# Optimization experiments

Measured on AMD Instinct MI355X. Metric: run time of the kernel, lower is better.

The kernel has to match this reference:

```python
import jax, jax.numpy as jnp
import numpy as np

B, S, H, D = 4, 2048, 16, 64
CAUSAL = True
NEG_INF = -1e30


def setup_inputs() -> dict:
    key = jax.random.key(0)
    k1, k2, k3, k4 = jax.random.split(key, 4)
    q = jax.random.normal(k1, (B, S, H, D), dtype=jnp.float32)
    k = jax.random.normal(k2, (B, S, H, D), dtype=jnp.float32)
    v = jax.random.normal(k3, (B, S, H, D), dtype=jnp.float32)
    bias = jax.random.normal(k4, (1, H, S, S), dtype=jnp.float32)
    return {"q": q, "k": k, "v": v, "bias": bias}


def reference(q, k, v, bias):
    # q,k,v: [B, S, H, D]; bias: [1, H, S, S] (broadcast over batch)
    scale = 1.0 / jnp.sqrt(jnp.asarray(D, dtype=q.dtype))
    # scores: [B, H, Sq, Sk]
    s = jnp.einsum('bqhd,bkhd->bhqk', q, k) * scale + bias
    if CAUSAL:
        causal_mask = jnp.tril(jnp.ones((S, S), dtype=bool))  # [Sq, Sk]
        s = jnp.where(causal_mask[None, None, :, :], s, NEG_INF)
    p = jax.nn.softmax(s, axis=-1)
    out = jnp.einsum('bhqk,bkhd->bqhd', p, v)  # [B, S, H, D]
    return out
```

## Files before the change

kernel.cpp:

```cpp
#include <hip/hip_runtime.h>

typedef __attribute__((ext_vector_type(8))) short short8;
typedef __attribute__((ext_vector_type(4))) float floatx4;

constexpr int kS = 2048, kH = 16, kD = 64;
constexpr int kBatch = 4;
constexpr float kScale = 0.125f;
constexpr int LSTR = 72;

__device__ inline unsigned short f2bf(float x) {
  unsigned u = __float_as_uint(x);
  u += 0x7fffu + ((u >> 16) & 1u);
  return (unsigned short)(u >> 16);
}

__device__ inline unsigned cvt_pk_bf16(float lo, float hi) {
  unsigned r;
  asm("v_cvt_pk_bf16_f32 %0, %1, %2" : "=v"(r) : "v"(lo), "v"(hi));
  return r;
}

__global__ __launch_bounds__(256) void prepass_kernel(
    const float* __restrict__ Q, const float* __restrict__ K,
    const float* __restrict__ V, unsigned short* __restrict__ Qb,
    unsigned short* __restrict__ Kb, unsigned short* __restrict__ Vt) {
  __shared__ unsigned short vs[64 * LSTR];
  const int t = threadIdx.x;
  const int st = blockIdx.x, h = blockIdx.y, b = blockIdx.z;
  const int bh = b * kH + h;
  const int r = t >> 2, c = (t & 3) * 16;
  const int s = st * 64 + r;
  const size_t in_off = ((size_t)(b * kS + s) * kH + h) * kD + c;
  const size_t qk_out = ((size_t)bh * kS + s) * kD + c;

  unsigned short tmp[16];
  {
    const float4* ip = (const float4*)(Q + in_off);
#pragma unroll
    for (int i = 0; i < 4; ++i) {
      float4 f = ip[i];
      tmp[i*4+0]=f2bf(f.x); tmp[i*4+1]=f2bf(f.y); tmp[i*4+2]=f2bf(f.z); tmp[i*4+3]=f2bf(f.w);
    }
    *(uint4*)(Qb + qk_out) = *(const uint4*)&tmp[0];
    *(uint4*)(Qb + qk_out + 8) = *(const uint4*)&tmp[8];
  }
  {
    const float4* ip = (const float4*)(K + in_off);
#pragma unroll
    for (int i = 0; i < 4; ++i) {
      float4 f = ip[i];
      tmp[i*4+0]=f2bf(f.x); tmp[i*4+1]=f2bf(f.y); tmp[i*4+2]=f2bf(f.z); tmp[i*4+3]=f2bf(f.w);
    }
    *(uint4*)(Kb + qk_out) = *(const uint4*)&tmp[0];
    *(uint4*)(Kb + qk_out + 8) = *(const uint4*)&tmp[8];
  }
  {
    const float4* ip = (const float4*)(V + in_off);
#pragma unroll
    for (int i = 0; i < 4; ++i) {
      float4 f = ip[i];
      tmp[i*4+0]=f2bf(f.x); tmp[i*4+1]=f2bf(f.y); tmp[i*4+2]=f2bf(f.z); tmp[i*4+3]=f2bf(f.w);
    }
    *(uint4*)&vs[r * LSTR + c] = *(const uint4*)&tmp[0];
    *(uint4*)&vs[r * LSTR + c + 8] = *(const uint4*)&tmp[8];
  }
  __syncthreads();
  unsigned short tv[16];
#pragma unroll
  for (int i = 0; i < 16; ++i) tv[i] = vs[(c + i) * LSTR + r];
  const size_t vt_out = ((size_t)bh * kD + r) * kS + st * 64 + c;
  *(uint4*)(Vt + vt_out) = *(const uint4*)&tv[0];
  *(uint4*)(Vt + vt_out + 8) = *(const uint4*)&tv[8];
}

__global__ __launch_bounds__(256, 3) void fa_mfma_kernel(
    const unsigned short* __restrict__ Qb, const unsigned short* __restrict__ Kb,
    const unsigned short* __restrict__ Vt, const float* __restrict__ Bias,
    float* __restrict__ O) {
  __shared__ unsigned short Ks[2][64 * LSTR];
  __shared__ unsigned short Vs[2][64 * LSTR];
  __shared__ unsigned short Ps[64 * LSTR];

  const int t = threadIdx.x;
  const int lane = t & 63, w = t >> 6;
  const int quad = lane >> 4, l16 = lane & 15;

  const int p = blockIdx.x;
  const int xcd = p & 7;
  const int r = p >> 3;
  const int qt = 31 - (r >> 3);
  const int b = (r >> 1) & 3;
  const int h = ((r & 1) << 3) | xcd;
  const int bh = b * kH + h;

  const int sr = t >> 2, sc = (t & 3) * 16;

  const int qrow = qt * 64 + w * 16 + l16;

  short8 aQ[2];
  {
    const unsigned short* qp = Qb + ((size_t)bh * kS + qrow) * kD + quad * 8;
    aQ[0] = *(const short8*)qp;
    aQ[1] = *(const short8*)(qp + 32);
  }

  unsigned short* Psw = Ps + w * 16 * LSTR;

  floatx4 acc[4];
#pragma unroll
  for (int i = 0; i < 4; ++i) acc[i] = (floatx4){0.f, 0.f, 0.f, 0.f};
  float lp = 0.f;

  const float* bp = Bias + (size_t)h * kS * kS + (size_t)qrow * kS + quad * 4;
  const unsigned short* Kbh = Kb + (size_t)bh * kS * kD;
  const unsigned short* Vbh = Vt + (size_t)bh * kD * kS;

  uint4 kr0, kr1, vr0, vr1;
  float4 bbA[4], bbB[4];

  {
    const uint4* srck = (const uint4*)(Kbh + (size_t)sr * kD + sc);
    kr0 = srck[0]; kr1 = srck[1];
    const uint4* srcv = (const uint4*)(Vbh + (size_t)sr * kS + sc);
    vr0 = srcv[0]; vr1 = srcv[1];
  }
#pragma unroll
  for (int nt = 0; nt < 4; ++nt) bbA[nt] = *(const float4*)(bp + nt * 16);
  *(uint4*)&Ks[0][sr * LSTR + sc] = kr0;
  *(uint4*)&Ks[0][sr * LSTR + sc + 8] = kr1;
  *(uint4*)&Vs[0][sr * LSTR + sc] = vr0;
  *(uint4*)&Vs[0][sr * LSTR + sc + 8] = vr1;
  if (qt > 0) {
    const uint4* srck = (const uint4*)(Kbh + (size_t)(64 + sr) * kD + sc);
    kr0 = srck[0]; kr1 = srck[1];
    const uint4* srcv = (const uint4*)(Vbh + (size_t)sr * kS + 64 + sc);
    vr0 = srcv[0]; vr1 = srcv[1];
#pragma unroll
    for (int nt = 0; nt < 4; ++nt) bbB[nt] = *(const float4*)(bp + 64 + nt * 16);
  }
  __syncthreads();

  auto iter = [&](const int kb, const unsigned short* Kc, const unsigned short* Vc,
                  unsigned short* Kn, unsigned short* Vn, float4* bb) {
    const int k0 = kb * 64;
    const bool diag = (kb == qt);

#pragma unroll
    for (int nt = 0; nt < 4; ++nt) {
      short8 a0 = *(const short8*)&Kc[(nt * 16 + l16) * LSTR + quad * 8];
      short8 a1 = *(const short8*)&Kc[(nt * 16 + l16) * LSTR + quad * 8 + 32];
      floatx4 cf = (floatx4){0.f, 0.f, 0.f, 0.f};
      cf = __builtin_amdgcn_mfma_f32_16x16x32_bf16(a0, aQ[0], cf, 0, 0, 0);
      cf = __builtin_amdgcn_mfma_f32_16x16x32_bf16(a1, aQ[1], cf, 0, 0, 0);
      const int colb = k0 + nt * 16 + quad * 4;
      const float* bf = (const float*)&bb[nt];
      float p4[4];
#pragma unroll
      for (int reg = 0; reg < 4; ++reg) {
        const float x = cf[reg] * kScale + bf[reg];
        float pv = __expf(x);
        if (diag && (colb + reg > qrow)) pv = 0.f;
        p4[reg] = pv;
      }
      lp += (p4[0] + p4[1]) + (p4[2] + p4[3]);
      const unsigned u0 = cvt_pk_bf16(p4[0], p4[1]);
      const unsigned u1 = cvt_pk_bf16(p4[2], p4[3]);
      *(uint2*)&Psw[l16 * LSTR + nt * 16 + quad * 4] = make_uint2(u0, u1);
    }

#pragma unroll
    for (int ks = 0; ks < 2; ++ks) {
      short8 aP = *(const short8*)&Psw[l16 * LSTR + ks * 32 + quad * 8];
#pragma unroll
      for (int dt = 0; dt < 4; ++dt) {
        short8 bV = *(const short8*)&Vc[(dt * 16 + l16) * LSTR + ks * 32 + quad * 8];
        acc[dt] = __builtin_amdgcn_mfma_f32_16x16x32_bf16(aP, bV, acc[dt], 0, 0, 0);
      }
    }

    if (kb < qt) {
      *(uint4*)&Kn[sr * LSTR + sc] = kr0;
      *(uint4*)&Kn[sr * LSTR + sc + 8] = kr1;
      *(uint4*)&Vn[sr * LSTR + sc] = vr0;
      *(uint4*)&Vn[sr * LSTR + sc + 8] = vr1;
      if (kb + 1 < qt) {
        const int kn = k0 + 128;
        const uint4* srck = (const uint4*)(Kbh + (size_t)(kn + sr) * kD + sc);
        kr0 = srck[0]; kr1 = srck[1];
        const uint4* srcv = (const uint4*)(Vbh + (size_t)sr * kS + kn + sc);
        vr0 = srcv[0]; vr1 = srcv[1];
#pragma unroll
        for (int nt = 0; nt < 4; ++nt) bb[nt] = *(const float4*)(bp + kn + nt * 16);
      }
      __syncthreads();
    }
  };

  for (int kb = 0; kb <= qt; kb += 2) {
    iter(kb, Ks[0], Vs[0], Ks[1], Vs[1], bbA);
    if (kb + 1 <= qt) iter(kb + 1, Ks[1], Vs[1], Ks[0], Vs[0], bbB);
  }

  lp += __shfl_xor(lp, 16, 64);
  lp += __shfl_xor(lp, 32, 64);
  const float linv = 1.f / lp;
#pragma unroll
  for (int reg = 0; reg < 4; ++reg) {
    const float il = __shfl(linv, quad * 4 + reg, 16);
    float* op = O + ((size_t)(b * kS + qt * 64 + w * 16 + quad * 4 + reg) * kH + h) * kD;
#pragma unroll
    for (int dt = 0; dt < 4; ++dt)
      op[dt * 16 + l16] = acc[dt][reg] * il;
  }
}

extern "C" void kernel_launch(void* const* d_in, const int* in_sizes, int n_in,
                              void* d_out, int out_size, void* d_ws, size_t ws_size,
                              hipStream_t stream) {
  const float* q = (const float*)d_in[0];
  const float* k = (const float*)d_in[1];
  const float* v = (const float*)d_in[2];
  const float* bias = (const float*)d_in[3];
  float* out = (float*)d_out;

  const size_t elems = (size_t)kBatch * kH * kS * kD;
  unsigned short* Qb = (unsigned short*)d_ws;
  unsigned short* Kb = Qb + elems;
  unsigned short* Vt = Kb + elems;

  dim3 pgrid(kS / 64, kH, kBatch);
  prepass_kernel<<<pgrid, dim3(256), 0, stream>>>(q, k, v, Qb, Kb, Vt);
  fa_mfma_kernel<<<dim3(32 * kH * kBatch), dim3(256), 0, stream>>>(Qb, Kb, Vt, bias, out);
}
```

Baseline: 488.0 us.

## Double query tile to 128 rows per block, reusing K/V tiles across two query groups

Each block now handles 128 query rows (32 per wave, as two 16-row groups) instead of 64, so every K/V tile loaded into shared memory feeds twice as many MFMAs. This halves K/V global and LDS traffic per query and the number of blocks. Waves whose rows lie entirely above a diagonal key tile now skip its compute. Register pressure roughly doubles (accumulators, bias prefetch), so launch bounds drop from 3 to 2 blocks per CU, and the coarser causal tiles give less even load balance.

Measured after the change: 494.8 us. No clear change (+1.4%).

```diff
diff --git a/kernel.cpp b/kernel.cpp
--- a/kernel.cpp
+++ b/kernel.cpp
@@ -73,13 +73,13 @@
   *(uint4*)(Vt + vt_out + 8) = *(const uint4*)&tv[8];
 }
 
-__global__ __launch_bounds__(256, 3) void fa_mfma_kernel(
+__global__ __launch_bounds__(256, 2) void fa_mfma_kernel(
     const unsigned short* __restrict__ Qb, const unsigned short* __restrict__ Kb,
     const unsigned short* __restrict__ Vt, const float* __restrict__ Bias,
     float* __restrict__ O) {
   __shared__ unsigned short Ks[2][64 * LSTR];
   __shared__ unsigned short Vs[2][64 * LSTR];
-  __shared__ unsigned short Ps[64 * LSTR];
+  __shared__ unsigned short Ps[128 * LSTR];
 
   const int t = threadIdx.x;
   const int lane = t & 63, w = t >> 6;
@@ -88,35 +88,44 @@
   const int p = blockIdx.x;
   const int xcd = p & 7;
   const int r = p >> 3;
-  const int qt = 31 - (r >> 3);
+  const int qt = 15 - (r >> 3);
   const int b = (r >> 1) & 3;
   const int h = ((r & 1) << 3) | xcd;
   const int bh = b * kH + h;
 
   const int sr = t >> 2, sc = (t & 3) * 16;
 
-  const int qrow = qt * 64 + w * 16 + l16;
-
-  short8 aQ[2];
-  {
-    const unsigned short* qp = Qb + ((size_t)bh * kS + qrow) * kD + quad * 8;
-    aQ[0] = *(const short8*)qp;
-    aQ[1] = *(const short8*)(qp + 32);
-  }
-
-  unsigned short* Psw = Ps + w * 16 * LSTR;
-
-  floatx4 acc[4];
-#pragma unroll
-  for (int i = 0; i < 4; ++i) acc[i] = (floatx4){0.f, 0.f, 0.f, 0.f};
-  float lp = 0.f;
-
-  const float* bp = Bias + (size_t)h * kS * kS + (size_t)qrow * kS + quad * 4;
+  const int qr0 = qt * 128 + w * 32 + l16;
+
+  short8 aQ[2][2];
+#pragma unroll
+  for (int qg = 0; qg < 2; ++qg) {
+    const unsigned short* qp = Qb + ((size_t)bh * kS + qr0 + qg * 16) * kD + quad * 8;
+    aQ[qg][0] = *(const short8*)qp;
+    aQ[qg][1] = *(const short8*)(qp + 32);
+  }
+
+  unsigned short* Psw = Ps + w * 32 * LSTR;
+
+  floatx4 acc[2][4];
+#pragma unroll
+  for (int qg = 0; qg < 2; ++qg)
+#pragma unroll
+    for (int i = 0; i < 4; ++i) acc[qg][i] = (floatx4){0.f, 0.f, 0.f, 0.f};
+  float lp[2] = {0.f, 0.f};
+
+  const float* bp[2];
+#pragma unroll
+  for (int qg = 0; qg < 2; ++qg)
+    bp[qg] = Bias + (size_t)h * kS * kS + (size_t)(qr0 + qg * 16) * kS + quad * 4;
   const unsigned short* Kbh = Kb + (size_t)bh * kS * kD;
   const unsigned short* Vbh = Vt + (size_t)bh * kD * kS;
 
+  const int nkb = 2 * qt + 2;
+  const int wmax = qt * 128 + w * 32 + 31;
+
   uint4 kr0, kr1, vr0, vr1;
-  float4 bbA[4], bbB[4];
+  float4 bbA[8], bbB[8];
 
   {
     const uint4* srck = (const uint4*)(Kbh + (size_t)sr * kD + sc);
@@ -125,92 +134,122 @@
     vr0 = srcv[0]; vr1 = srcv[1];
   }
 #pragma unroll
-  for (int nt = 0; nt < 4; ++nt) bbA[nt] = *(const float4*)(bp + nt * 16);
+  for (int qg = 0; qg < 2; ++qg)
+#pragma unroll
+    for (int nt = 0; nt < 4; ++nt) bbA[qg * 4 + nt] = *(const float4*)(bp[qg] + nt * 16);
   *(uint4*)&Ks[0][sr * LSTR + sc] = kr0;
   *(uint4*)&Ks[0][sr * LSTR + sc + 8] = kr1;
   *(uint4*)&Vs[0][sr * LSTR + sc] = vr0;
   *(uint4*)&Vs[0][sr * LSTR + sc + 8] = vr1;
-  if (qt > 0) {
+  {
     const uint4* srck = (const uint4*)(Kbh + (size_t)(64 + sr) * kD + sc);
     kr0 = srck[0]; kr1 = srck[1];
     const uint4* srcv = (const uint4*)(Vbh + (size_t)sr * kS + 64 + sc);
     vr0 = srcv[0]; vr1 = srcv[1];
 #pragma unroll
-    for (int nt = 0; nt < 4; ++nt) bbB[nt] = *(const float4*)(bp + 64 + nt * 16);
+    for (int qg = 0; qg < 2; ++qg)
+#pragma unroll
+      for (int nt = 0; nt < 4; ++nt) bbB[qg * 4 + nt] = *(const float4*)(bp[qg] + 64 + nt * 16);
   }
   __syncthreads();
 
   auto iter = [&](const int kb, const unsigned short* Kc, const unsigned short* Vc,
                   unsigned short* Kn, unsigned short* Vn, float4* bb) {
     const int k0 = kb * 64;
-    const bool diag = (kb == qt);
-
-#pragma unroll
-    for (int nt = 0; nt < 4; ++nt) {
-      short8 a0 = *(const short8*)&Kc[(nt * 16 + l16) * LSTR + quad * 8];
-      short8 a1 = *(const short8*)&Kc[(nt * 16 + l16) * LSTR + quad * 8 + 32];
-      floatx4 cf = (floatx4){0.f, 0.f, 0.f, 0.f};
-      cf = __builtin_amdgcn_mfma_f32_16x16x32_bf16(a0, aQ[0], cf, 0, 0, 0);
-      cf = __builtin_amdgcn_mfma_f32_16x16x32_bf16(a1, aQ[1], cf, 0, 0, 0);
-      const int colb = k0 + nt * 16 + quad * 4;
-      const float* bf = (const float*)&bb[nt];
-      float p4[4];
-#pragma unroll
-      for (int reg = 0; reg < 4; ++reg) {
-        const float x = cf[reg] * kScale + bf[reg];
-        float pv = __expf(x);
-        if (diag && (colb + reg > qrow)) pv = 0.f;
-        p4[reg] = pv;
+    const bool diag = (kb >= 2 * qt);
+    const bool alive = !(diag && (k0 > wmax));
+
+    if (alive) {
+#pragma unroll
+      for (int nt = 0; nt < 4; ++nt) {
+        short8 a0 = *(const short8*)&Kc[(nt * 16 + l16) * LSTR + quad * 8];
+        short8 a1 = *(const short8*)&Kc[(nt * 16 + l16) * LSTR + quad * 8 + 32];
+        floatx4 cf[2];
+#pragma unroll
+        for (int qg = 0; qg < 2; ++qg) {
+          floatx4 c0 = (floatx4){0.f, 0.f, 0.f, 0.f};
+          c0 = __builtin_amdgcn_mfma_f32_16x16x32_bf16(a0, aQ[qg][0], c0, 0, 0, 0);
+          cf[qg] = __builtin_amdgcn_mfma_f32_16x16x32_bf16(a1, aQ[qg][1], c0, 0, 0, 0);
+        }
+        const int colb = k0 + nt * 16 + quad * 4;
+#pragma unroll
+        for (int qg = 0; qg < 2; ++qg) {
+          const float* bf = (const float*)&bb[qg * 4 + nt];
+          const int qrow = qr0 + qg * 16;
+          float p4[4];
+#pragma unroll
+          for (int reg = 0; reg < 4; ++reg) {
+            const float x = cf[qg][reg] * kScale + bf[reg];
+            float pv = __expf(x);
+            if (diag && (colb + reg > qrow)) pv = 0.f;
+            p4[reg] = pv;
+          }
+          lp[qg] += (p4[0] + p4[1]) + (p4[2] + p4[3]);
+          const unsigned u0 = cvt_pk_bf16(p4[0], p4[1]);
+          const unsigned u1 = cvt_pk_bf16(p4[2], p4[3]);
+          *(uint2*)&Psw[(qg * 16 + l16) * LSTR + nt * 16 + quad * 4] = make_uint2(u0, u1);
+        }
       }
-      lp += (p4[0] + p4[1]) + (p4[2] + p4[3]);
-      const unsigned u0 = cvt_pk_bf16(p4[0], p4[1]);
-      const unsigned u1 = cvt_pk_bf16(p4[2], p4[3]);
-      *(uint2*)&Psw[l16 * LSTR + nt * 16 + quad * 4] = make_uint2(u0, u1);
-    }
-
-#pragma unroll
-    for (int ks = 0; ks < 2; ++ks) {
-      short8 aP = *(const short8*)&Psw[l16 * LSTR + ks * 32 + quad * 8];
-#pragma unroll
-      for (int dt = 0; dt < 4; ++dt) {
-        short8 bV = *(const short8*)&Vc[(dt * 16 + l16) * LSTR + ks * 32 + quad * 8];
-        acc[dt] = __builtin_amdgcn_mfma_f32_16x16x32_bf16(aP, bV, acc[dt], 0, 0, 0);
+    }
+
+    if (kb + 2 < nkb) {
+      const int kn = k0 + 128;
+#pragma unroll
+      for (int qg = 0; qg < 2; ++qg)
+#pragma unroll
+        for (int nt = 0; nt < 4; ++nt)
+          bb[qg * 4 + nt] = *(const float4*)(bp[qg] + kn + nt * 16);
+    }
+
+    if (alive) {
+#pragma unroll
+      for (int ks = 0; ks < 2; ++ks) {
+        short8 aP0 = *(const short8*)&Psw[l16 * LSTR + ks * 32 + quad * 8];
+        short8 aP1 = *(const short8*)&Psw[(16 + l16) * LSTR + ks * 32 + quad * 8];
+#pragma unroll
+        for (int dt = 0; dt < 4; ++dt) {
+          short8 bV = *(const short8*)&Vc[(dt * 16 + l16) * LSTR + ks * 32 + quad * 8];
+          acc[0][dt] = __builtin_amdgcn_mfma_f32_16x16x32_bf16(aP0, bV, acc[0][dt], 0, 0, 0);
+          acc[1][dt] = __builtin_amdgcn_mfma_f32_16x16x32_bf16(aP1, bV, acc[1][dt], 0, 0, 0);
+        }
       }
     }
 
-    if (kb < qt) {
+    if (kb + 1 < nkb) {
       *(uint4*)&Kn[sr * LSTR + sc] = kr0;
       *(uint4*)&Kn[sr * LSTR + sc + 8] = kr1;
       *(uint4*)&Vn[sr * LSTR + sc] = vr0;
       *(uint4*)&Vn[sr * LSTR + sc + 8] = vr1;
-      if (kb + 1 < qt) {
+      if (kb + 2 < nkb) {
         const int kn = k0 + 128;
         const uint4* srck = (const uint4*)(Kbh + (size_t)(kn + sr) * kD + sc);
         kr0 = srck[0]; kr1 = srck[1];
         const uint4* srcv = (const uint4*)(Vbh + (size_t)sr * kS + kn + sc);
         vr0 = srcv[0]; vr1 = srcv[1];
-#pragma unroll
-        for (int nt = 0; nt < 4; ++nt) bb[nt] = *(const float4*)(bp + kn + nt * 16);
       }
       __syncthreads();
     }
   };
 
-  for (int kb = 0; kb <= qt; kb += 2) {
+  for (int kb = 0; kb < nkb; kb += 2) {
     iter(kb, Ks[0], Vs[0], Ks[1], Vs[1], bbA);
-    if (kb + 1 <= qt) iter(kb + 1, Ks[1], Vs[1], Ks[0], Vs[0], bbB);
-  }
-
-  lp += __shfl_xor(lp, 16, 64);
-  lp += __shfl_xor(lp, 32, 64);
-  const float linv = 1.f / lp;
-#pragma unroll
-  for (int reg = 0; reg < 4; ++reg) {
-    const float il = __shfl(linv, quad * 4 + reg, 16);
-    float* op = O + ((size_t)(b * kS + qt * 64 + w * 16 + quad * 4 + reg) * kH + h) * kD;
-#pragma unroll
-    for (int dt = 0; dt < 4; ++dt)
-      op[dt * 16 + l16] = acc[dt][reg] * il;
+    iter(kb + 1, Ks[1], Vs[1], Ks[0], Vs[0], bbB);
+  }
+
+#pragma unroll
+  for (int qg = 0; qg < 2; ++qg) {
+    float l = lp[qg];
+    l += __shfl_xor(l, 16, 64);
+    l += __shfl_xor(l, 32, 64);
+    const float linv = 1.f / l;
+#pragma unroll
+    for (int reg = 0; reg < 4; ++reg) {
+      const float il = __shfl(linv, quad * 4 + reg, 16);
+      float* op = O + ((size_t)(b * kS + qt * 128 + w * 32 + qg * 16 + quad * 4 + reg) * kH + h) * kD;
+#pragma unroll
+      for (int dt = 0; dt < 4; ++dt)
+        op[dt * 16 + l16] = acc[qg][dt][reg] * il;
+    }
   }
 }
 
@@ -230,5 +269,5 @@
 
   dim3 pgrid(kS / 64, kH, kBatch);
   prepass_kernel<<<pgrid, dim3(256), 0, stream>>>(q, k, v, Qb, Kb, Vt);
-  fa_mfma_kernel<<<dim3(32 * kH * kBatch), dim3(256), 0, stream>>>(Qb, Kb, Vt, bias, out);
-}
+  fa_mfma_kernel<<<dim3((kS / 128) * kH * kBatch), dim3(256), 0, stream>>>(Qb, Kb, Vt, bias, out);
+}
```
